# Kernel tuning notes

Hardware: AMD Instinct MI355X
Metric: run time of the kernel (lower is better)

Reference implementation:

```python
import jax, jax.numpy as jnp
import numpy as np

TAU = 2.0          # LIF membrane time constant (init kwarg)
ALPHA = 2.0        # spikingjelly surrogate.ATan default alpha
V_TH = 1.0         # spikingjelly LIFNode default v_threshold

# Heaviside spike with ATan surrogate gradient (spikingjelly semantics)
@jax.custom_vjp
def spike(v):
    return (v >= V_TH).astype(v.dtype)

def _spike_fwd(v):
    return spike(v), v

def _spike_bwd(v, g):
    sg = (ALPHA / 2.0) / (1.0 + (jnp.pi / 2.0 * ALPHA * (v - V_TH)) ** 2)
    return (g * sg,)

spike.defvjp(_spike_fwd, _spike_bwd)

def lif(x):
    # Fresh LIFNode: v_prev = 0, v_reset = 0, decay_input=True
    # charge: v = v_prev + (x - (v_prev - v_reset)) / tau  ->  v = x / tau
    return spike(x / TAU)

def setup_inputs() -> dict:
    key = jax.random.key(0)
    ks = jax.random.split(key, 5)
    B = 2097152
    # kaiming-uniform-ish scale: 1/sqrt(fan_in)
    def w(k, out_f, in_f):
        return jax.random.normal(k, (out_f, in_f), dtype=jnp.float32) / np.sqrt(in_f)
    return {
        "x": jax.random.normal(ks[0], (B, 5), dtype=jnp.float32),
        "W1": w(ks[1], 32, 5),
        "W2": w(ks[2], 32, 32),
        "W3": w(ks[3], 16, 32),
        "W4": w(ks[4], 10, 16),
    }

def reference(x, W1, W2, W3, W4):
    # fc: Linear(5,32)->LIF -> Linear(32,32)->LIF -> Linear(32,16)->LIF
    s = lif(x @ W1.T)          # [B, 32]
    s = lif(s @ W2.T)          # [B, 32]
    s = lif(s @ W3.T)          # [B, 16]
    # fc1: Linear(16,10)->LIF
    return lif(s @ W4.T)       # [B, 10]
```

## Files before the change

kernel.cpp:

```cpp
#include <hip/hip_runtime.h>


typedef float v4f __attribute__((ext_vector_type(4)));

#define RPB 512

__global__ __launch_bounds__(256) void snn_fused(
    const float* __restrict__ x,
    const float* __restrict__ W1,
    const float* __restrict__ W2,
    const float* __restrict__ W3,
    const float* __restrict__ W4,
    float* __restrict__ out,
    int B)
{
    __shared__ float buf[RPB * 10];
    __shared__ float w2t[32 * 36];

    const int t = threadIdx.x;
    const long base = (long)blockIdx.x * RPB;
    const int nrows = (int)min((long)RPB, (long)B - base);

#pragma unroll
    for (int e = t; e < 1024; e += 256) {
        int j = e >> 5, i = e & 31;
        w2t[i * 36 + j] = W2[e];
    }

    if (nrows == RPB) {
        const v4f* xg = (const v4f*)(x + base * 5);
        v4f* b4 = (v4f*)buf;
#pragma unroll
        for (int e = 0; e < 3; ++e) {
            int idx = e * 256 + t;
            if (idx < (RPB * 5) / 4) b4[idx] = xg[idx];
        }
    } else {
        for (int e = t; e < nrows * 5; e += 256) buf[e] = x[base * 5 + e];
    }
    __syncthreads();

    float xr[2][5];
#pragma unroll
    for (int c = 0; c < 2; ++c) {
        int lr = c * 256 + t;
        if (lr < nrows) {
#pragma unroll
            for (int k = 0; k < 5; ++k) xr[c][k] = buf[lr * 5 + k];
        }
    }
    __syncthreads();

#pragma unroll
    for (int c = 0; c < 2; ++c) {
        int lr = c * 256 + t;
        if (lr >= nrows) continue;

        unsigned m = 0u;
#pragma unroll
        for (int j = 0; j < 32; ++j) {
            const float* w = W1 + j * 5;
            float h = xr[c][0] * w[0];
            h += xr[c][1] * w[1];
            h += xr[c][2] * w[2];
            h += xr[c][3] * w[3];
            h += xr[c][4] * w[4];
            if (h >= 2.0f) m |= (1u << j);
        }

        float o[10];
#pragma unroll
        for (int j = 0; j < 10; ++j) o[j] = 0.0f;

        if (m) {
            float h[32];
#pragma unroll
            for (int j = 0; j < 32; ++j) h[j] = 0.0f;
            unsigned mm = m;
            while (mm) {
                int i = __ffs(mm) - 1;
                mm &= mm - 1;
                const float* wr = &w2t[i * 36];
#pragma unroll
                for (int j = 0; j < 32; ++j) h[j] += wr[j];
            }
            unsigned m2 = 0u;
#pragma unroll
            for (int j = 0; j < 32; ++j)
                if (h[j] >= 2.0f) m2 |= (1u << j);

            if (m2) {
                unsigned m3 = 0u;
#pragma unroll
                for (int j = 0; j < 16; ++j) {
                    float g = 0.0f;
#pragma unroll
                    for (int i = 0; i < 32; ++i)
                        if ((m2 >> i) & 1u) g += W3[j * 32 + i];
                    if (g >= 2.0f) m3 |= (1u << j);
                }
#pragma unroll
                for (int j = 0; j < 10; ++j) {
                    float g = 0.0f;
#pragma unroll
                    for (int i = 0; i < 16; ++i)
                        if ((m3 >> i) & 1u) g += W4[j * 16 + i];
                    o[j] = (g >= 2.0f) ? 1.0f : 0.0f;
                }
            }
        }

#pragma unroll
        for (int j = 0; j < 10; ++j) buf[lr * 10 + j] = o[j];
    }
    __syncthreads();

    if (nrows == RPB) {
        v4f* og = (v4f*)(out + base * 10);
        const v4f* b4 = (const v4f*)buf;
#pragma unroll
        for (int e = 0; e < 5; ++e) {
            int idx = e * 256 + t;
            __builtin_nontemporal_store(b4[idx], &og[idx]);
        }
    } else {
        for (int e = t; e < nrows * 10; e += 256) out[base * 10 + e] = buf[e];
    }
}

extern "C" void kernel_launch(void* const* d_in, const int* in_sizes, int n_in,
                              void* d_out, int out_size, void* d_ws, size_t ws_size,
                              hipStream_t stream) {
    const float* x  = (const float*)d_in[0];
    const float* W1 = (const float*)d_in[1];
    const float* W2 = (const float*)d_in[2];
    const float* W3 = (const float*)d_in[3];
    const float* W4 = (const float*)d_in[4];
    float* out = (float*)d_out;

    int B = in_sizes[0] / 5;
    int grid = (B + RPB - 1) / RPB;
    snn_fused<<<grid, 256, 0, stream>>>(x, W1, W2, W3, W4, out, B);
}
```

Before: 141.2 us.

## Skip deeper layers via W2 max-weight bound and pack two rows per thread

Result: slower. 163.1 us (+15.5%).

```diff
diff --git a/kernel.cpp b/kernel.cpp
--- a/kernel.cpp
+++ b/kernel.cpp
@@ -1,6 +1,7 @@
 #include <hip/hip_runtime.h>
 
 
+typedef float v2f __attribute__((ext_vector_type(2)));
 typedef float v4f __attribute__((ext_vector_type(4)));
 
 #define RPB 512
@@ -14,18 +15,26 @@
     float* __restrict__ out,
     int B)
 {
-    __shared__ float buf[RPB * 10];
+    __shared__ __align__(16) float buf[RPB * 10];
     __shared__ float w2t[32 * 36];
+    __shared__ unsigned s_gmax;
 
     const int t = threadIdx.x;
     const long base = (long)blockIdx.x * RPB;
     const int nrows = (int)min((long)RPB, (long)B - base);
 
+    if (t == 0) s_gmax = 0u;
+    __syncthreads();
+
+    float lmax = 0.0f;
 #pragma unroll
     for (int e = t; e < 1024; e += 256) {
         int j = e >> 5, i = e & 31;
-        w2t[i * 36 + j] = W2[e];
+        float w = W2[e];
+        w2t[i * 36 + j] = w;
+        lmax = fmaxf(lmax, w);
     }
+    if (lmax > 0.0f) atomicMax(&s_gmax, __float_as_uint(lmax));
 
     if (nrows == RPB) {
         const v4f* xg = (const v4f*)(x + base * 5);
@@ -40,39 +49,48 @@
     }
     __syncthreads();
 
-    float xr[2][5];
+    const float gmax = __uint_as_float(s_gmax);
+
+    v2f X[5];
+    {
+        int rA = t, rB = 256 + t;
+        int a = (rA < nrows) ? rA : 0;
+        int b = (rB < nrows) ? rB : a;
 #pragma unroll
-    for (int c = 0; c < 2; ++c) {
-        int lr = c * 256 + t;
-        if (lr < nrows) {
-#pragma unroll
-            for (int k = 0; k < 5; ++k) xr[c][k] = buf[lr * 5 + k];
-        }
+        for (int k = 0; k < 5; ++k) X[k] = (v2f){ buf[a * 5 + k], buf[b * 5 + k] };
     }
     __syncthreads();
+
+    if (nrows == RPB) {
+        v4f* b4 = (v4f*)buf;
+        const v4f z = { 0.f, 0.f, 0.f, 0.f };
+#pragma unroll
+        for (int e = 0; e < 5; ++e) b4[e * 256 + t] = z;
+    } else {
+        for (int e = t; e < nrows * 10; e += 256) buf[e] = 0.0f;
+    }
+    __syncthreads();
+
+    unsigned mA = 0u, mB = 0u;
+#pragma unroll
+    for (int j = 0; j < 32; ++j) {
+        const float* w = W1 + j * 5;
+        v2f h = X[0] * w[0];
+        h += X[1] * w[1];
+        h += X[2] * w[2];
+        h += X[3] * w[3];
+        h += X[4] * w[4];
+        if (h.x >= 2.0f) mA |= (1u << j);
+        if (h.y >= 2.0f) mB |= (1u << j);
+    }
 
 #pragma unroll
     for (int c = 0; c < 2; ++c) {
         int lr = c * 256 + t;
         if (lr >= nrows) continue;
-
-        unsigned m = 0u;
-#pragma unroll
-        for (int j = 0; j < 32; ++j) {
-            const float* w = W1 + j * 5;
-            float h = xr[c][0] * w[0];
-            h += xr[c][1] * w[1];
-            h += xr[c][2] * w[2];
-            h += xr[c][3] * w[3];
-            h += xr[c][4] * w[4];
-            if (h >= 2.0f) m |= (1u << j);
-        }
-
-        float o[10];
-#pragma unroll
-        for (int j = 0; j < 10; ++j) o[j] = 0.0f;
-
-        if (m) {
+        unsigned m = c ? mB : mA;
+        float bound = (float)__popc(m) * gmax;
+        if (bound >= 1.99f) {
             float h[32];
 #pragma unroll
             for (int j = 0; j < 32; ++j) h[j] = 0.0f;
@@ -99,6 +117,7 @@
                         if ((m2 >> i) & 1u) g += W3[j * 32 + i];
                     if (g >= 2.0f) m3 |= (1u << j);
                 }
+                float o[10];
 #pragma unroll
                 for (int j = 0; j < 10; ++j) {
                     float g = 0.0f;
@@ -107,11 +126,11 @@
                         if ((m3 >> i) & 1u) g += W4[j * 16 + i];
                     o[j] = (g >= 2.0f) ? 1.0f : 0.0f;
                 }
+                v2f* bp = (v2f*)&buf[lr * 10];
+#pragma unroll
+                for (int q = 0; q < 5; ++q) bp[q] = (v2f){ o[2 * q], o[2 * q + 1] };
             }
         }
-
-#pragma unroll
-        for (int j = 0; j < 10; ++j) buf[lr * 10 + j] = o[j];
     }
     __syncthreads();
 
```

## Halve rows per block, add max-weight early-out bound, vectorize layer-2 accumulation

Applied to the files above, without the earlier changes.

Measured after the change: 145.4 us. 3.0% more time.

```diff
diff --git a/kernel.cpp b/kernel.cpp
--- a/kernel.cpp
+++ b/kernel.cpp
@@ -3,7 +3,7 @@
 
 typedef float v4f __attribute__((ext_vector_type(4)));
 
-#define RPB 512
+#define RPB 256
 
 __global__ __launch_bounds__(256) void snn_fused(
     const float* __restrict__ x,
@@ -14,80 +14,87 @@
     float* __restrict__ out,
     int B)
 {
-    __shared__ float buf[RPB * 10];
+    __shared__ __align__(16) float xs[RPB * 5];
+    __shared__ __align__(16) float os[RPB * 10];
     __shared__ float w2t[32 * 36];
+    __shared__ float red[4];
 
     const int t = threadIdx.x;
     const long base = (long)blockIdx.x * RPB;
     const int nrows = (int)min((long)RPB, (long)B - base);
 
+    float lmax = 0.0f;
 #pragma unroll
     for (int e = t; e < 1024; e += 256) {
         int j = e >> 5, i = e & 31;
-        w2t[i * 36 + j] = W2[e];
+        float w = W2[e];
+        w2t[i * 36 + j] = w;
+        lmax = fmaxf(lmax, w);
     }
+#pragma unroll
+    for (int k = 1; k < 64; k <<= 1)
+        lmax = fmaxf(lmax, __shfl_xor(lmax, k, 64));
+    if ((t & 63) == 0) red[t >> 6] = lmax;
 
     if (nrows == RPB) {
         const v4f* xg = (const v4f*)(x + base * 5);
-        v4f* b4 = (v4f*)buf;
+        v4f* xs4 = (v4f*)xs;
+#pragma unroll
+        for (int e = 0; e < 2; ++e) {
+            int idx = e * 256 + t;
+            if (idx < (RPB * 5) / 4) xs4[idx] = xg[idx];
+        }
+    } else {
+        for (int e = t; e < nrows * 5; e += 256) xs[e] = x[base * 5 + e];
+    }
+    {
+        v4f* os4 = (v4f*)os;
+        const v4f z = { 0.f, 0.f, 0.f, 0.f };
 #pragma unroll
         for (int e = 0; e < 3; ++e) {
             int idx = e * 256 + t;
-            if (idx < (RPB * 5) / 4) b4[idx] = xg[idx];
-        }
-    } else {
-        for (int e = t; e < nrows * 5; e += 256) buf[e] = x[base * 5 + e];
-    }
-    __syncthreads();
-
-    float xr[2][5];
-#pragma unroll
-    for (int c = 0; c < 2; ++c) {
-        int lr = c * 256 + t;
-        if (lr < nrows) {
-#pragma unroll
-            for (int k = 0; k < 5; ++k) xr[c][k] = buf[lr * 5 + k];
+            if (idx < (RPB * 10) / 4) os4[idx] = z;
         }
     }
     __syncthreads();
 
-#pragma unroll
-    for (int c = 0; c < 2; ++c) {
-        int lr = c * 256 + t;
-        if (lr >= nrows) continue;
+    const float gmax = fmaxf(fmaxf(red[0], red[1]), fmaxf(red[2], red[3]));
+
+    if (t < nrows) {
+        const float* xp = &xs[t * 5];
+        float x0 = xp[0], x1 = xp[1], x2 = xp[2], x3 = xp[3], x4 = xp[4];
 
         unsigned m = 0u;
 #pragma unroll
         for (int j = 0; j < 32; ++j) {
             const float* w = W1 + j * 5;
-            float h = xr[c][0] * w[0];
-            h += xr[c][1] * w[1];
-            h += xr[c][2] * w[2];
-            h += xr[c][3] * w[3];
-            h += xr[c][4] * w[4];
+            float h = x0 * w[0];
+            h += x1 * w[1];
+            h += x2 * w[2];
+            h += x3 * w[3];
+            h += x4 * w[4];
             if (h >= 2.0f) m |= (1u << j);
         }
 
-        float o[10];
+        if ((float)__popc(m) * gmax >= 1.99f) {
+            v4f h4[8];
 #pragma unroll
-        for (int j = 0; j < 10; ++j) o[j] = 0.0f;
-
-        if (m) {
-            float h[32];
-#pragma unroll
-            for (int j = 0; j < 32; ++j) h[j] = 0.0f;
+            for (int q = 0; q < 8; ++q) h4[q] = (v4f){0.f, 0.f, 0.f, 0.f};
             unsigned mm = m;
             while (mm) {
                 int i = __ffs(mm) - 1;
                 mm &= mm - 1;
-                const float* wr = &w2t[i * 36];
+                const v4f* wr = (const v4f*)&w2t[i * 36];
 #pragma unroll
-                for (int j = 0; j < 32; ++j) h[j] += wr[j];
+                for (int q = 0; q < 8; ++q) h4[q] += wr[q];
             }
             unsigned m2 = 0u;
 #pragma unroll
-            for (int j = 0; j < 32; ++j)
-                if (h[j] >= 2.0f) m2 |= (1u << j);
+            for (int q = 0; q < 8; ++q) {
+#pragma unroll
+                for (int r = 0; r < 4; ++r)
+                    if (h4[q][r] >= 2.0f) m2 |= (1u << (q * 4 + r));
+            }
 
             if (m2) {
                 unsigned m3 = 0u;
@@ -105,26 +112,24 @@
 #pragma unroll
                     for (int i = 0; i < 16; ++i)
                         if ((m3 >> i) & 1u) g += W4[j * 16 + i];
-                    o[j] = (g >= 2.0f) ? 1.0f : 0.0f;
+                    os[t * 10 + j] = (g >= 2.0f) ? 1.0f : 0.0f;
                 }
             }
         }
-
-#pragma unroll
-        for (int j = 0; j < 10; ++j) buf[lr * 10 + j] = o[j];
     }
     __syncthreads();
 
     if (nrows == RPB) {
         v4f* og = (v4f*)(out + base * 10);
-        const v4f* b4 = (const v4f*)buf;
+        const v4f* os4 = (const v4f*)os;
 #pragma unroll
-        for (int e = 0; e < 5; ++e) {
+        for (int e = 0; e < 3; ++e) {
             int idx = e * 256 + t;
-            __builtin_nontemporal_store(b4[idx], &og[idx]);
+            if (idx < (RPB * 10) / 4)
+                __builtin_nontemporal_store(os4[idx], &og[idx]);
         }
     } else {
-        for (int e = t; e < nrows * 10; e += 256) out[base * 10 + e] = buf[e];
+        for (int e = t; e < nrows * 10; e += 256) out[base * 10 + e] = os[e];
     }
 }
 
```
